# Kernel optimization log

Hardware: AMD Instinct MI355X
Metric: run time of the kernel (lower is better)

Reference implementation:

```python
import jax, jax.numpy as jnp
import numpy as np

N_NODES = 1_000_000
N_EDGES = 32_000_000


def setup_inputs() -> dict:
    key = jax.random.key(0)
    k1, k2, k3 = jax.random.split(key, 3)
    x = jax.random.normal(k1, (N_NODES, 4), dtype=jnp.float32)
    edge_index = jax.random.randint(k2, (2, N_EDGES), 0, N_NODES, dtype=jnp.int64)
    # edge_attr holds inter-node distances in the PINN setting; keep strictly positive
    edge_attr = jax.random.uniform(k3, (N_EDGES, 2), dtype=jnp.float32, minval=0.1, maxval=1.0)
    return {"x": x, "edge_index": edge_index, "edge_attr": edge_attr}


def reference(x, edge_index, edge_attr):
    # SpatialDerivativeOperator with index_derivative_node=0, index_derivative_edge=0
    nodes_input = x[:, 0]            # [N]
    edges_input = edge_attr[:, 0]    # [E]

    src_idx = edge_index[0]          # [E]
    dst_idx = edge_index[1]          # [E]

    # EdgeSpatialDerivative: (dest - src) / edge_attr
    src = nodes_input[src_idx]       # gather [E]
    dest = nodes_input[dst_idx]      # gather [E]
    local_derivative = (dest - src) / edges_input  # [E]

    # NodeSpatialDerivative: scatter_mean over destination index, dim_size = N
    n = x.shape[0]
    seg_sum = jax.ops.segment_sum(local_derivative, dst_idx, num_segments=n)
    seg_cnt = jax.ops.segment_sum(jnp.ones_like(local_derivative), dst_idx, num_segments=n)
    # scatter_mean returns 0 for nodes with no incoming edges
    derivative = jnp.where(seg_cnt > 0, seg_sum / jnp.maximum(seg_cnt, 1.0), 0.0)
    return derivative  # [N]
```

## Files before the change

kernel.cpp:

```cpp
#include <hip/hip_runtime.h>


typedef float          f32x2 __attribute__((ext_vector_type(2)));
typedef float          f32x4 __attribute__((ext_vector_type(4)));
typedef unsigned short u16x4 __attribute__((ext_vector_type(4)));

#define SDO_SCALE     8388608.0f
#define RSCALE        8192.0f
#define NBKT_BITS     11
#define NODES_PER_BKT 2048
#define TILE          16384
#define BLOCK_BIN     1024
#define EPT           16
#define NB_MAX        512
#define CAP           68000u


__global__ void sdo_init(const float* __restrict__ x, float* __restrict__ x0,
                         unsigned int* __restrict__ cursor, int n_nodes, int nb) {
    int i = blockIdx.x * blockDim.x + threadIdx.x;
    if (i < n_nodes) x0[i] = x[4 * i];
    if (i < nb) cursor[i] = (unsigned int)i * CAP;
}

__global__ __launch_bounds__(BLOCK_BIN, 4) void sdo_bin(
        const int* __restrict__ src_idx, const int* __restrict__ dst_idx,
        const float* __restrict__ x0, const float* __restrict__ edge_attr,
        float* __restrict__ ebuf_val, unsigned short* __restrict__ ebuf_idx,
        unsigned int* __restrict__ cursor, int n_edges, int nb) {
    __shared__ float          stage_val[TILE];
    __shared__ unsigned short stage_idx[TILE];
    __shared__ unsigned int hist[NB_MAX];
    __shared__ unsigned int scanA[NB_MAX];
    __shared__ unsigned int base_l[NB_MAX];
    __shared__ unsigned int base_g[NB_MAX];
    __shared__ unsigned int cnt2[NB_MAX];

    const int tid = threadIdx.x;
    const long long tbase = (long long)blockIdx.x * TILE;

    if (tid < NB_MAX) { hist[tid] = 0u; cnt2[tid] = 0u; }
    __syncthreads();

    int   dreg[EPT], sreg[EPT];
    float areg[EPT];
    #pragma unroll
    for (int k = 0; k < EPT; ++k) {
        long long e = tbase + (long long)k * BLOCK_BIN + tid;
        bool ok = (e < n_edges);
        dreg[k] = ok ? __builtin_nontemporal_load(&dst_idx[e]) : -1;
        sreg[k] = ok ? __builtin_nontemporal_load(&src_idx[e]) : 0;
        f32x2 a2 = ok ? __builtin_nontemporal_load((const f32x2*)edge_attr + e)
                      : (f32x2){1.0f, 1.0f};
        areg[k] = a2.x;
    }

    float gd[EPT], gs[EPT];
    #pragma unroll
    for (int k = 0; k < EPT; ++k) gd[k] = x0[dreg[k] < 0 ? 0 : dreg[k]];
    #pragma unroll
    for (int k = 0; k < EPT; ++k) gs[k] = x0[sreg[k]];

    float vreg[EPT];
    #pragma unroll
    for (int k = 0; k < EPT; ++k) {
        vreg[k] = (gd[k] - gs[k]) / areg[k];
        if (dreg[k] >= 0) atomicAdd(&hist[dreg[k] >> NBKT_BITS], 1u);
    }
    __syncthreads();

    if (tid < NB_MAX) scanA[tid] = hist[tid];
    __syncthreads();
    for (int off = 1; off < NB_MAX; off <<= 1) {
        unsigned int v = 0;
        if (tid < NB_MAX && tid >= off) v = scanA[tid - off];
        __syncthreads();
        if (tid < NB_MAX) scanA[tid] += v;
        __syncthreads();
    }
    if (tid < NB_MAX) {
        base_l[tid] = scanA[tid] - hist[tid];
        unsigned int c = hist[tid];
        base_g[tid] = c ? atomicAdd(&cursor[tid], c) : 0u;
    }
    __syncthreads();

    #pragma unroll
    for (int k = 0; k < EPT; ++k) {
        int d = dreg[k];
        if (d >= 0) {
            int b = d >> NBKT_BITS;
            unsigned int r = atomicAdd(&cnt2[b], 1u);
            unsigned int idx = base_l[b] + r;
            stage_val[idx] = vreg[k];
            stage_idx[idx] = (unsigned short)(d & (NODES_PER_BKT - 1));
        }
    }
    __syncthreads();

    const unsigned int total = scanA[NB_MAX - 1];
    for (unsigned int j = tid; j < total; j += BLOCK_BIN) {
        int lo = 0;
        #pragma unroll
        for (int step = 256; step >= 1; step >>= 1) {
            int mid = lo + step;
            if (mid < NB_MAX && base_l[mid] <= j) lo = mid;
        }
        unsigned int g = base_g[lo] + (j - base_l[lo]);
        __builtin_nontemporal_store(stage_val[j], &ebuf_val[g]);
        __builtin_nontemporal_store(stage_idx[j], &ebuf_idx[g]);
    }
}

__global__ __launch_bounds__(1024) void sdo_reduce(
        const float* __restrict__ ebuf_val,
        const unsigned short* __restrict__ ebuf_idx,
        const unsigned int* __restrict__ cursor,
        float* __restrict__ out, int n_nodes) {
    __shared__ unsigned int acc[NODES_PER_BKT];
    const int b = blockIdx.x;
    const int tid = threadIdx.x;
    if (tid < NODES_PER_BKT) acc[tid] = 0u;
    if (tid + 1024 < NODES_PER_BKT) acc[tid + 1024] = 0u;
    __syncthreads();

    const unsigned int beg = (unsigned int)b * CAP;
    const unsigned int end = cursor[b];
    const unsigned int n   = end - beg;
    const unsigned int n4  = n >> 2;

    const f32x4* v4 = (const f32x4*)(ebuf_val + beg);
    const u16x4* i4 = (const u16x4*)(ebuf_idx + beg);
    for (unsigned int t = tid; t < n4; t += 1024) {
        f32x4 v  = __builtin_nontemporal_load(&v4[t]);
        u16x4 ii = __builtin_nontemporal_load(&i4[t]);
        int q0 = __float2int_rn(v.x * RSCALE);
        int q1 = __float2int_rn(v.y * RSCALE);
        int q2 = __float2int_rn(v.z * RSCALE);
        int q3 = __float2int_rn(v.w * RSCALE);
        atomicAdd(&acc[ii.x], ((unsigned int)q0 << 8) + 1u);
        atomicAdd(&acc[ii.y], ((unsigned int)q1 << 8) + 1u);
        atomicAdd(&acc[ii.z], ((unsigned int)q2 << 8) + 1u);
        atomicAdd(&acc[ii.w], ((unsigned int)q3 << 8) + 1u);
    }
    for (unsigned int j = beg + (n4 << 2) + tid; j < end; j += 1024) {
        float v = ebuf_val[j];
        int d_low = ebuf_idx[j];
        int q = __float2int_rn(v * RSCALE);
        atomicAdd(&acc[d_low], ((unsigned int)q << 8) + 1u);
    }
    __syncthreads();

    const int nbase = b << NBKT_BITS;
    for (int i = tid; i < NODES_PER_BKT; i += 1024) {
        int node = nbase + i;
        if (node < n_nodes) {
            int t = (int)acc[i];
            int cnt = t & 0xFF;
            int sf  = t >> 8;
            out[node] = cnt ? ((float)sf / RSCALE) / (float)cnt : 0.0f;
        }
    }
}


__global__ void sdo_scatter_packed_strided(const int* __restrict__ src_idx,
                                           const int* __restrict__ dst_idx,
                                           const float* __restrict__ x,
                                           const float* __restrict__ edge_attr,
                                           unsigned long long* __restrict__ packed,
                                           int n_edges) {
    int i = blockIdx.x * blockDim.x + threadIdx.x;
    if (i >= n_edges) return;
    int s = src_idx[i];
    int d = dst_idx[i];
    float e  = edge_attr[2 * i];
    float ld = (x[4 * d] - x[4 * s]) / e;
    long long q = __float2ll_rn(ld * SDO_SCALE);
    atomicAdd(&packed[d], (unsigned long long)((q << 20) + 1));
}

__global__ void sdo_finalize_packed(const unsigned long long* __restrict__ packed,
                                    float* __restrict__ out, int n_nodes) {
    int i = blockIdx.x * blockDim.x + threadIdx.x;
    if (i >= n_nodes) return;
    long long t = (long long)packed[i];
    long long cnt = t & 0xFFFFFLL;
    long long sf  = t >> 20;
    out[i] = (cnt > 0) ? (float)(((double)sf / (double)SDO_SCALE) / (double)cnt) : 0.0f;
}


extern "C" void kernel_launch(void* const* d_in, const int* in_sizes, int n_in,
                              void* d_out, int out_size, void* d_ws, size_t ws_size,
                              hipStream_t stream) {
    const float* x         = (const float*)d_in[0];
    const int*   edge_idx  = (const int*)d_in[1];
    const float* edge_attr = (const float*)d_in[2];

    const int n_nodes = in_sizes[0] / 4;
    const int n_edges = in_sizes[2] / 2;
    const int* src_idx = edge_idx;
    const int* dst_idx = edge_idx + n_edges;
    float* out = (float*)d_out;

    const int nb = (n_nodes + NODES_PER_BKT - 1) >> NBKT_BITS;

    const size_t eval_bytes = (size_t)nb * CAP * sizeof(float);
    const size_t eidx_bytes = (size_t)nb * CAP * sizeof(unsigned short);
    const size_t x0_bytes   = (size_t)n_nodes * sizeof(float);
    const size_t cur_bytes  = (size_t)nb * sizeof(unsigned int);
    const size_t need_full  = eval_bytes + eidx_bytes + x0_bytes + cur_bytes;

    const int block = 256;

    if (ws_size >= need_full && nb <= NB_MAX) {
        float* ebuf_val = (float*)d_ws;
        unsigned short* ebuf_idx = (unsigned short*)((char*)d_ws + eval_bytes);
        float* x0 = (float*)((char*)d_ws + eval_bytes + eidx_bytes);
        unsigned int* cursor =
            (unsigned int*)((char*)d_ws + eval_bytes + eidx_bytes + x0_bytes);

        const int grid_init = (n_nodes + block - 1) / block;
        sdo_init<<<grid_init, block, 0, stream>>>(x, x0, cursor, n_nodes, nb);

        const int grid_bin = (n_edges + TILE - 1) / TILE;
        sdo_bin<<<grid_bin, BLOCK_BIN, 0, stream>>>(src_idx, dst_idx, x0, edge_attr,
                                                    ebuf_val, ebuf_idx, cursor,
                                                    n_edges, nb);

        sdo_reduce<<<nb, 1024, 0, stream>>>(ebuf_val, ebuf_idx, cursor, out, n_nodes);
    } else {
        unsigned long long* packed = (unsigned long long*)d_ws;
        (void)hipMemsetAsync(packed, 0, (size_t)n_nodes * sizeof(unsigned long long), stream);
        const int grid_e = (n_edges + block - 1) / block;
        sdo_scatter_packed_strided<<<grid_e, block, 0, stream>>>(
            src_idx, dst_idx, x, edge_attr, packed, n_edges);
        const int grid_n = (n_nodes + block - 1) / block;
        sdo_finalize_packed<<<grid_n, block, 0, stream>>>(packed, out, n_nodes);
    }
}
```

Measured before the change: 978.5 us.

## Split edge value computation from binning and reuse histogram ranks for scatter

Edge derivative values are now computed in a separate high-occupancy kernel that writes them to a temporary buffer, and the binning kernel reads those values instead of doing the random gathers itself. The binning kernel keeps the rank returned by the histogram atomic, which removes the second atomic counter pass, and stores the bucket id with each staged entry so the write-out no longer needs a binary search. The reduce kernel also software-prefetches its next vector load. The split adds an extra 128 MB write and read of values, in exchange for hiding gather latency better than the large 1024-thread binning block can. When the workspace is too small for the temporary buffer, a fused fallback runs instead.

```diff
diff --git a/kernel.cpp b/kernel.cpp
--- a/kernel.cpp
+++ b/kernel.cpp
@@ -14,6 +14,7 @@
 #define EPT           16
 #define NB_MAX        512
 #define CAP           68000u
+#define EPV           8
 
 
 __global__ void sdo_init(const float* __restrict__ x, float* __restrict__ x0,
@@ -23,49 +24,66 @@
     if (i < nb) cursor[i] = (unsigned int)i * CAP;
 }
 
-__global__ __launch_bounds__(BLOCK_BIN, 4) void sdo_bin(
+__global__ __launch_bounds__(256, 4) void sdo_val(
         const int* __restrict__ src_idx, const int* __restrict__ dst_idx,
         const float* __restrict__ x0, const float* __restrict__ edge_attr,
+        float* __restrict__ vtmp, int n_edges) {
+    const long long base = (long long)blockIdx.x * (256 * EPV) + threadIdx.x;
+    int   d[EPV], s[EPV];
+    float a[EPV];
+    #pragma unroll
+    for (int k = 0; k < EPV; ++k) {
+        long long e = base + (long long)k * 256;
+        bool ok = (e < n_edges);
+        d[k] = ok ? __builtin_nontemporal_load(&dst_idx[e]) : 0;
+        s[k] = ok ? __builtin_nontemporal_load(&src_idx[e]) : 0;
+        f32x2 a2 = ok ? __builtin_nontemporal_load((const f32x2*)edge_attr + e)
+                      : (f32x2){1.0f, 1.0f};
+        a[k] = a2.x;
+    }
+    float gd[EPV], gs[EPV];
+    #pragma unroll
+    for (int k = 0; k < EPV; ++k) gd[k] = x0[d[k]];
+    #pragma unroll
+    for (int k = 0; k < EPV; ++k) gs[k] = x0[s[k]];
+    #pragma unroll
+    for (int k = 0; k < EPV; ++k) {
+        long long e = base + (long long)k * 256;
+        if (e < n_edges)
+            __builtin_nontemporal_store((gd[k] - gs[k]) / a[k], &vtmp[e]);
+    }
+}
+
+__global__ __launch_bounds__(BLOCK_BIN, 4) void sdo_bin2(
+        const int* __restrict__ dst_idx, const float* __restrict__ vtmp,
         float* __restrict__ ebuf_val, unsigned short* __restrict__ ebuf_idx,
         unsigned int* __restrict__ cursor, int n_edges, int nb) {
-    __shared__ float          stage_val[TILE];
-    __shared__ unsigned short stage_idx[TILE];
+    __shared__ float        stage_val[TILE];
+    __shared__ unsigned int stage_meta[TILE];
     __shared__ unsigned int hist[NB_MAX];
     __shared__ unsigned int scanA[NB_MAX];
     __shared__ unsigned int base_l[NB_MAX];
     __shared__ unsigned int base_g[NB_MAX];
-    __shared__ unsigned int cnt2[NB_MAX];
 
     const int tid = threadIdx.x;
     const long long tbase = (long long)blockIdx.x * TILE;
 
-    if (tid < NB_MAX) { hist[tid] = 0u; cnt2[tid] = 0u; }
-    __syncthreads();
-
-    int   dreg[EPT], sreg[EPT];
-    float areg[EPT];
+    if (tid < NB_MAX) hist[tid] = 0u;
+    __syncthreads();
+
+    int          dreg[EPT];
+    float        vreg[EPT];
+    unsigned int rreg[EPT];
     #pragma unroll
     for (int k = 0; k < EPT; ++k) {
         long long e = tbase + (long long)k * BLOCK_BIN + tid;
-        bool ok = (e < n_edges);
-        dreg[k] = ok ? __builtin_nontemporal_load(&dst_idx[e]) : -1;
-        sreg[k] = ok ? __builtin_nontemporal_load(&src_idx[e]) : 0;
-        f32x2 a2 = ok ? __builtin_nontemporal_load((const f32x2*)edge_attr + e)
-                      : (f32x2){1.0f, 1.0f};
-        areg[k] = a2.x;
-    }
-
-    float gd[EPT], gs[EPT];
-    #pragma unroll
-    for (int k = 0; k < EPT; ++k) gd[k] = x0[dreg[k] < 0 ? 0 : dreg[k]];
-    #pragma unroll
-    for (int k = 0; k < EPT; ++k) gs[k] = x0[sreg[k]];
-
-    float vreg[EPT];
-    #pragma unroll
-    for (int k = 0; k < EPT; ++k) {
-        vreg[k] = (gd[k] - gs[k]) / areg[k];
-        if (dreg[k] >= 0) atomicAdd(&hist[dreg[k] >> NBKT_BITS], 1u);
+        if (e < n_edges) {
+            dreg[k] = __builtin_nontemporal_load(&dst_idx[e]);
+            vreg[k] = __builtin_nontemporal_load(&vtmp[e]);
+            rreg[k] = atomicAdd(&hist[dreg[k] >> NBKT_BITS], 1u);
+        } else {
+            dreg[k] = -1;
+        }
     }
     __syncthreads();
 
@@ -90,25 +108,22 @@
         int d = dreg[k];
         if (d >= 0) {
             int b = d >> NBKT_BITS;
-            unsigned int r = atomicAdd(&cnt2[b], 1u);
-            unsigned int idx = base_l[b] + r;
-            stage_val[idx] = vreg[k];
-            stage_idx[idx] = (unsigned short)(d & (NODES_PER_BKT - 1));
+            unsigned int idx = base_l[b] + rreg[k];
+            stage_val[idx]  = vreg[k];
+            stage_meta[idx] = ((unsigned int)b << NBKT_BITS)
+                            | (unsigned int)(d & (NODES_PER_BKT - 1));
         }
     }
     __syncthreads();
 
     const unsigned int total = scanA[NB_MAX - 1];
     for (unsigned int j = tid; j < total; j += BLOCK_BIN) {
-        int lo = 0;
-        #pragma unroll
-        for (int step = 256; step >= 1; step >>= 1) {
-            int mid = lo + step;
-            if (mid < NB_MAX && base_l[mid] <= j) lo = mid;
-        }
-        unsigned int g = base_g[lo] + (j - base_l[lo]);
+        unsigned int m = stage_meta[j];
+        unsigned int b = m >> NBKT_BITS;
+        unsigned int g = base_g[b] + (j - base_l[b]);
         __builtin_nontemporal_store(stage_val[j], &ebuf_val[g]);
-        __builtin_nontemporal_store(stage_idx[j], &ebuf_idx[g]);
+        __builtin_nontemporal_store((unsigned short)(m & (NODES_PER_BKT - 1)),
+                                    &ebuf_idx[g]);
     }
 }
 
@@ -120,8 +135,8 @@
     __shared__ unsigned int acc[NODES_PER_BKT];
     const int b = blockIdx.x;
     const int tid = threadIdx.x;
-    if (tid < NODES_PER_BKT) acc[tid] = 0u;
-    if (tid + 1024 < NODES_PER_BKT) acc[tid + 1024] = 0u;
+    acc[tid] = 0u;
+    acc[tid + 1024] = 0u;
     __syncthreads();
 
     const unsigned int beg = (unsigned int)b * CAP;
@@ -131,17 +146,26 @@
 
     const f32x4* v4 = (const f32x4*)(ebuf_val + beg);
     const u16x4* i4 = (const u16x4*)(ebuf_idx + beg);
-    for (unsigned int t = tid; t < n4; t += 1024) {
-        f32x4 v  = __builtin_nontemporal_load(&v4[t]);
-        u16x4 ii = __builtin_nontemporal_load(&i4[t]);
-        int q0 = __float2int_rn(v.x * RSCALE);
-        int q1 = __float2int_rn(v.y * RSCALE);
-        int q2 = __float2int_rn(v.z * RSCALE);
-        int q3 = __float2int_rn(v.w * RSCALE);
-        atomicAdd(&acc[ii.x], ((unsigned int)q0 << 8) + 1u);
-        atomicAdd(&acc[ii.y], ((unsigned int)q1 << 8) + 1u);
-        atomicAdd(&acc[ii.z], ((unsigned int)q2 << 8) + 1u);
-        atomicAdd(&acc[ii.w], ((unsigned int)q3 << 8) + 1u);
+
+    f32x4 va; u16x4 ia;
+    unsigned int t = tid;
+    if (t < n4) { va = __builtin_nontemporal_load(&v4[t]);
+                  ia = __builtin_nontemporal_load(&i4[t]); }
+    for (; t < n4; ) {
+        unsigned int tn = t + 1024;
+        f32x4 vb; u16x4 ib;
+        if (tn < n4) { vb = __builtin_nontemporal_load(&v4[tn]);
+                       ib = __builtin_nontemporal_load(&i4[tn]); }
+        int q0 = __float2int_rn(va.x * RSCALE);
+        int q1 = __float2int_rn(va.y * RSCALE);
+        int q2 = __float2int_rn(va.z * RSCALE);
+        int q3 = __float2int_rn(va.w * RSCALE);
+        atomicAdd(&acc[ia.x], ((unsigned int)q0 << 8) + 1u);
+        atomicAdd(&acc[ia.y], ((unsigned int)q1 << 8) + 1u);
+        atomicAdd(&acc[ia.z], ((unsigned int)q2 << 8) + 1u);
+        atomicAdd(&acc[ia.w], ((unsigned int)q3 << 8) + 1u);
+        va = vb; ia = ib;
+        t = tn;
     }
     for (unsigned int j = beg + (n4 << 2) + tid; j < end; j += 1024) {
         float v = ebuf_val[j];
@@ -155,11 +179,89 @@
     for (int i = tid; i < NODES_PER_BKT; i += 1024) {
         int node = nbase + i;
         if (node < n_nodes) {
-            int t = (int)acc[i];
-            int cnt = t & 0xFF;
-            int sf  = t >> 8;
+            int tt = (int)acc[i];
+            int cnt = tt & 0xFF;
+            int sf  = tt >> 8;
             out[node] = cnt ? ((float)sf / RSCALE) / (float)cnt : 0.0f;
         }
+    }
+}
+
+
+__global__ __launch_bounds__(BLOCK_BIN, 4) void sdo_bin_fused(
+        const int* __restrict__ src_idx, const int* __restrict__ dst_idx,
+        const float* __restrict__ x0, const float* __restrict__ edge_attr,
+        float* __restrict__ ebuf_val, unsigned short* __restrict__ ebuf_idx,
+        unsigned int* __restrict__ cursor, int n_edges, int nb) {
+    __shared__ float        stage_val[TILE];
+    __shared__ unsigned int stage_meta[TILE];
+    __shared__ unsigned int hist[NB_MAX];
+    __shared__ unsigned int scanA[NB_MAX];
+    __shared__ unsigned int base_l[NB_MAX];
+    __shared__ unsigned int base_g[NB_MAX];
+
+    const int tid = threadIdx.x;
+    const long long tbase = (long long)blockIdx.x * TILE;
+
+    if (tid < NB_MAX) hist[tid] = 0u;
+    __syncthreads();
+
+    int          dreg[EPT];
+    float        vreg[EPT];
+    unsigned int rreg[EPT];
+    #pragma unroll
+    for (int k = 0; k < EPT; ++k) {
+        long long e = tbase + (long long)k * BLOCK_BIN + tid;
+        if (e < n_edges) {
+            int d = __builtin_nontemporal_load(&dst_idx[e]);
+            int s = __builtin_nontemporal_load(&src_idx[e]);
+            f32x2 a2 = __builtin_nontemporal_load((const f32x2*)edge_attr + e);
+            dreg[k] = d;
+            vreg[k] = (x0[d] - x0[s]) / a2.x;
+            rreg[k] = atomicAdd(&hist[d >> NBKT_BITS], 1u);
+        } else {
+            dreg[k] = -1;
+        }
+    }
+    __syncthreads();
+
+    if (tid < NB_MAX) scanA[tid] = hist[tid];
+    __syncthreads();
+    for (int off = 1; off < NB_MAX; off <<= 1) {
+        unsigned int v = 0;
+        if (tid < NB_MAX && tid >= off) v = scanA[tid - off];
+        __syncthreads();
+        if (tid < NB_MAX) scanA[tid] += v;
+        __syncthreads();
+    }
+    if (tid < NB_MAX) {
+        base_l[tid] = scanA[tid] - hist[tid];
+        unsigned int c = hist[tid];
+        base_g[tid] = c ? atomicAdd(&cursor[tid], c) : 0u;
+    }
+    __syncthreads();
+
+    #pragma unroll
+    for (int k = 0; k < EPT; ++k) {
+        int d = dreg[k];
+        if (d >= 0) {
+            int b = d >> NBKT_BITS;
+            unsigned int idx = base_l[b] + rreg[k];
+            stage_val[idx]  = vreg[k];
+            stage_meta[idx] = ((unsigned int)b << NBKT_BITS)
+                            | (unsigned int)(d & (NODES_PER_BKT - 1));
+        }
+    }
+    __syncthreads();
+
+    const unsigned int total = scanA[NB_MAX - 1];
+    for (unsigned int j = tid; j < total; j += BLOCK_BIN) {
+        unsigned int m = stage_meta[j];
+        unsigned int b = m >> NBKT_BITS;
+        unsigned int g = base_g[b] + (j - base_l[b]);
+        __builtin_nontemporal_store(stage_val[j], &ebuf_val[g]);
+        __builtin_nontemporal_store((unsigned short)(m & (NODES_PER_BKT - 1)),
+                                    &ebuf_idx[g]);
     }
 }
 
@@ -209,8 +311,10 @@
     const size_t eval_bytes = (size_t)nb * CAP * sizeof(float);
     const size_t eidx_bytes = (size_t)nb * CAP * sizeof(unsigned short);
     const size_t x0_bytes   = (size_t)n_nodes * sizeof(float);
-    const size_t cur_bytes  = (size_t)nb * sizeof(unsigned int);
+    const size_t cur_bytes  = (size_t)((nb + 63) & ~63) * sizeof(unsigned int);
     const size_t need_full  = eval_bytes + eidx_bytes + x0_bytes + cur_bytes;
+    const size_t vtmp_bytes = (size_t)n_edges * sizeof(float);
+    const size_t need_split = need_full + vtmp_bytes;
 
     const int block = 256;
 
@@ -220,15 +324,24 @@
         float* x0 = (float*)((char*)d_ws + eval_bytes + eidx_bytes);
         unsigned int* cursor =
             (unsigned int*)((char*)d_ws + eval_bytes + eidx_bytes + x0_bytes);
+        float* vtmp = (float*)((char*)d_ws + need_full);
 
         const int grid_init = (n_nodes + block - 1) / block;
         sdo_init<<<grid_init, block, 0, stream>>>(x, x0, cursor, n_nodes, nb);
 
         const int grid_bin = (n_edges + TILE - 1) / TILE;
-        sdo_bin<<<grid_bin, BLOCK_BIN, 0, stream>>>(src_idx, dst_idx, x0, edge_attr,
-                                                    ebuf_val, ebuf_idx, cursor,
-                                                    n_edges, nb);
-
+        if (ws_size >= need_split) {
+            const int grid_val = (n_edges + block * EPV - 1) / (block * EPV);
+            sdo_val<<<grid_val, block, 0, stream>>>(src_idx, dst_idx, x0,
+                                                    edge_attr, vtmp, n_edges);
+            sdo_bin2<<<grid_bin, BLOCK_BIN, 0, stream>>>(dst_idx, vtmp,
+                                                         ebuf_val, ebuf_idx,
+                                                         cursor, n_edges, nb);
+        } else {
+            sdo_bin_fused<<<grid_bin, BLOCK_BIN, 0, stream>>>(
+                src_idx, dst_idx, x0, edge_attr,
+                ebuf_val, ebuf_idx, cursor, n_edges, nb);
+        }
         sdo_reduce<<<nb, 1024, 0, stream>>>(ebuf_val, ebuf_idx, cursor, out, n_nodes);
     } else {
         unsigned long long* packed = (unsigned long long*)d_ws;
```

After: 1.041 ms. 6.3% more time.

## Reuse histogram atomic ranks, store bucket id per staged edge, prefetch in reduce

Applied to the files above, without the earlier changes.

The binning kernel now keeps the return value of the histogram atomic as each edge's rank inside its bucket. This removes the second round of shared-memory atomics on a separate counter array. Each staged edge also stores its bucket id next to its local node index, so the scatter-out loop reads the bucket directly instead of doing a binary search over bucket offsets. The reduce kernel software-prefetches the next vector load before doing the shared atomics, and the per-edge load/gather/compute is merged into one loop, which may reduce how much independent memory work is in flight. The stage metadata array grows from 16-bit to 32-bit entries, adding shared memory.

```diff
diff --git a/kernel.cpp b/kernel.cpp
--- a/kernel.cpp
+++ b/kernel.cpp
@@ -23,49 +23,40 @@
     if (i < nb) cursor[i] = (unsigned int)i * CAP;
 }
 
-__global__ __launch_bounds__(BLOCK_BIN, 4) void sdo_bin(
+__global__ __launch_bounds__(BLOCK_BIN, 4) void sdo_bin3(
         const int* __restrict__ src_idx, const int* __restrict__ dst_idx,
         const float* __restrict__ x0, const float* __restrict__ edge_attr,
         float* __restrict__ ebuf_val, unsigned short* __restrict__ ebuf_idx,
         unsigned int* __restrict__ cursor, int n_edges, int nb) {
-    __shared__ float          stage_val[TILE];
-    __shared__ unsigned short stage_idx[TILE];
+    __shared__ float        stage_val[TILE];
+    __shared__ unsigned int stage_meta[TILE];
     __shared__ unsigned int hist[NB_MAX];
     __shared__ unsigned int scanA[NB_MAX];
     __shared__ unsigned int base_l[NB_MAX];
     __shared__ unsigned int base_g[NB_MAX];
-    __shared__ unsigned int cnt2[NB_MAX];
 
     const int tid = threadIdx.x;
     const long long tbase = (long long)blockIdx.x * TILE;
 
-    if (tid < NB_MAX) { hist[tid] = 0u; cnt2[tid] = 0u; }
-    __syncthreads();
-
-    int   dreg[EPT], sreg[EPT];
-    float areg[EPT];
+    if (tid < NB_MAX) hist[tid] = 0u;
+    __syncthreads();
+
+    int          dreg[EPT];
+    float        vreg[EPT];
+    unsigned int rreg[EPT];
     #pragma unroll
     for (int k = 0; k < EPT; ++k) {
         long long e = tbase + (long long)k * BLOCK_BIN + tid;
-        bool ok = (e < n_edges);
-        dreg[k] = ok ? __builtin_nontemporal_load(&dst_idx[e]) : -1;
-        sreg[k] = ok ? __builtin_nontemporal_load(&src_idx[e]) : 0;
-        f32x2 a2 = ok ? __builtin_nontemporal_load((const f32x2*)edge_attr + e)
-                      : (f32x2){1.0f, 1.0f};
-        areg[k] = a2.x;
-    }
-
-    float gd[EPT], gs[EPT];
-    #pragma unroll
-    for (int k = 0; k < EPT; ++k) gd[k] = x0[dreg[k] < 0 ? 0 : dreg[k]];
-    #pragma unroll
-    for (int k = 0; k < EPT; ++k) gs[k] = x0[sreg[k]];
-
-    float vreg[EPT];
-    #pragma unroll
-    for (int k = 0; k < EPT; ++k) {
-        vreg[k] = (gd[k] - gs[k]) / areg[k];
-        if (dreg[k] >= 0) atomicAdd(&hist[dreg[k] >> NBKT_BITS], 1u);
+        if (e < n_edges) {
+            int d = __builtin_nontemporal_load(&dst_idx[e]);
+            int s = __builtin_nontemporal_load(&src_idx[e]);
+            f32x2 a2 = __builtin_nontemporal_load((const f32x2*)edge_attr + e);
+            dreg[k] = d;
+            vreg[k] = (x0[d] - x0[s]) / a2.x;
+            rreg[k] = atomicAdd(&hist[d >> NBKT_BITS], 1u);
+        } else {
+            dreg[k] = -1;
+        }
     }
     __syncthreads();
 
@@ -90,25 +81,22 @@
         int d = dreg[k];
         if (d >= 0) {
             int b = d >> NBKT_BITS;
-            unsigned int r = atomicAdd(&cnt2[b], 1u);
-            unsigned int idx = base_l[b] + r;
-            stage_val[idx] = vreg[k];
-            stage_idx[idx] = (unsigned short)(d & (NODES_PER_BKT - 1));
+            unsigned int idx = base_l[b] + rreg[k];
+            stage_val[idx]  = vreg[k];
+            stage_meta[idx] = ((unsigned int)b << NBKT_BITS)
+                            | (unsigned int)(d & (NODES_PER_BKT - 1));
         }
     }
     __syncthreads();
 
     const unsigned int total = scanA[NB_MAX - 1];
     for (unsigned int j = tid; j < total; j += BLOCK_BIN) {
-        int lo = 0;
-        #pragma unroll
-        for (int step = 256; step >= 1; step >>= 1) {
-            int mid = lo + step;
-            if (mid < NB_MAX && base_l[mid] <= j) lo = mid;
-        }
-        unsigned int g = base_g[lo] + (j - base_l[lo]);
+        unsigned int m = stage_meta[j];
+        unsigned int b = m >> NBKT_BITS;
+        unsigned int g = base_g[b] + (j - base_l[b]);
         __builtin_nontemporal_store(stage_val[j], &ebuf_val[g]);
-        __builtin_nontemporal_store(stage_idx[j], &ebuf_idx[g]);
+        __builtin_nontemporal_store((unsigned short)(m & (NODES_PER_BKT - 1)),
+                                    &ebuf_idx[g]);
     }
 }
 
@@ -120,8 +108,8 @@
     __shared__ unsigned int acc[NODES_PER_BKT];
     const int b = blockIdx.x;
     const int tid = threadIdx.x;
-    if (tid < NODES_PER_BKT) acc[tid] = 0u;
-    if (tid + 1024 < NODES_PER_BKT) acc[tid + 1024] = 0u;
+    acc[tid] = 0u;
+    acc[tid + 1024] = 0u;
     __syncthreads();
 
     const unsigned int beg = (unsigned int)b * CAP;
@@ -131,17 +119,26 @@
 
     const f32x4* v4 = (const f32x4*)(ebuf_val + beg);
     const u16x4* i4 = (const u16x4*)(ebuf_idx + beg);
-    for (unsigned int t = tid; t < n4; t += 1024) {
-        f32x4 v  = __builtin_nontemporal_load(&v4[t]);
-        u16x4 ii = __builtin_nontemporal_load(&i4[t]);
-        int q0 = __float2int_rn(v.x * RSCALE);
-        int q1 = __float2int_rn(v.y * RSCALE);
-        int q2 = __float2int_rn(v.z * RSCALE);
-        int q3 = __float2int_rn(v.w * RSCALE);
-        atomicAdd(&acc[ii.x], ((unsigned int)q0 << 8) + 1u);
-        atomicAdd(&acc[ii.y], ((unsigned int)q1 << 8) + 1u);
-        atomicAdd(&acc[ii.z], ((unsigned int)q2 << 8) + 1u);
-        atomicAdd(&acc[ii.w], ((unsigned int)q3 << 8) + 1u);
+
+    f32x4 va; u16x4 ia;
+    unsigned int t = tid;
+    if (t < n4) { va = __builtin_nontemporal_load(&v4[t]);
+                  ia = __builtin_nontemporal_load(&i4[t]); }
+    for (; t < n4; ) {
+        unsigned int tn = t + 1024;
+        f32x4 vb; u16x4 ib;
+        if (tn < n4) { vb = __builtin_nontemporal_load(&v4[tn]);
+                       ib = __builtin_nontemporal_load(&i4[tn]); }
+        int q0 = __float2int_rn(va.x * RSCALE);
+        int q1 = __float2int_rn(va.y * RSCALE);
+        int q2 = __float2int_rn(va.z * RSCALE);
+        int q3 = __float2int_rn(va.w * RSCALE);
+        atomicAdd(&acc[ia.x], ((unsigned int)q0 << 8) + 1u);
+        atomicAdd(&acc[ia.y], ((unsigned int)q1 << 8) + 1u);
+        atomicAdd(&acc[ia.z], ((unsigned int)q2 << 8) + 1u);
+        atomicAdd(&acc[ia.w], ((unsigned int)q3 << 8) + 1u);
+        va = vb; ia = ib;
+        t = tn;
     }
     for (unsigned int j = beg + (n4 << 2) + tid; j < end; j += 1024) {
         float v = ebuf_val[j];
@@ -155,9 +152,9 @@
     for (int i = tid; i < NODES_PER_BKT; i += 1024) {
         int node = nbase + i;
         if (node < n_nodes) {
-            int t = (int)acc[i];
-            int cnt = t & 0xFF;
-            int sf  = t >> 8;
+            int tt = (int)acc[i];
+            int cnt = tt & 0xFF;
+            int sf  = tt >> 8;
             out[node] = cnt ? ((float)sf / RSCALE) / (float)cnt : 0.0f;
         }
     }
@@ -209,7 +206,7 @@
     const size_t eval_bytes = (size_t)nb * CAP * sizeof(float);
     const size_t eidx_bytes = (size_t)nb * CAP * sizeof(unsigned short);
     const size_t x0_bytes   = (size_t)n_nodes * sizeof(float);
-    const size_t cur_bytes  = (size_t)nb * sizeof(unsigned int);
+    const size_t cur_bytes  = (size_t)((nb + 63) & ~63) * sizeof(unsigned int);
     const size_t need_full  = eval_bytes + eidx_bytes + x0_bytes + cur_bytes;
 
     const int block = 256;
@@ -225,9 +222,10 @@
         sdo_init<<<grid_init, block, 0, stream>>>(x, x0, cursor, n_nodes, nb);
 
         const int grid_bin = (n_edges + TILE - 1) / TILE;
-        sdo_bin<<<grid_bin, BLOCK_BIN, 0, stream>>>(src_idx, dst_idx, x0, edge_attr,
-                                                    ebuf_val, ebuf_idx, cursor,
-                                                    n_edges, nb);
+        sdo_bin3<<<grid_bin, BLOCK_BIN, 0, stream>>>(src_idx, dst_idx, x0,
+                                                     edge_attr, ebuf_val,
+                                                     ebuf_idx, cursor,
+                                                     n_edges, nb);
 
         sdo_reduce<<<nb, 1024, 0, stream>>>(ebuf_val, ebuf_idx, cursor, out, n_nodes);
     } else {
```

Measured after the change: 1.022 ms. 1.04x slower.
